# Performance work log

Measured on AMD Instinct MI355X. Metric: run time of the kernel, lower is better.

Reference implementation:

```python
import jax, jax.numpy as jnp
import numpy as np

V, I_DIM, H_DIM, NUM_CLASSES = 32000, 300, 300, 3
B, T = 64, 128


def setup_inputs() -> dict:
    key = jax.random.key(0)
    ks = jax.random.split(key, 32)
    def g(k, shape, s=0.05):
        return (jax.random.normal(k, shape, jnp.float32) * s)
    linputs = jax.random.randint(ks[0], (B, T), 0, V)
    rinputs = jax.random.randint(ks[1], (B, T), 0, V)
    # strictly-lower-triangular binary child masks (children processed before parents)
    tril = jnp.tril(jnp.ones((T, T), jnp.float32), k=-1)
    lgraph = (jax.random.uniform(ks[2], (B, T, T)) < 0.05).astype(jnp.float32) * tril
    rgraph = (jax.random.uniform(ks[3], (B, T, T)) < 0.05).astype(jnp.float32) * tril
    emb = g(ks[4], (V, I_DIM), 0.02).at[0].set(0.0)  # padding_idx=0
    names = ['wi', 'wf', 'wo', 'wu', 'ui', 'uf', 'uo', 'uu']
    params = {}
    for n, (kw, kb) in zip(names, [(ks[5 + 2 * i], ks[6 + 2 * i]) for i in range(8)]):
        params[n + '_w'] = g(kw, (H_DIM, I_DIM if n[0] == 'w' else H_DIM))
        params[n + '_b'] = g(kb, (H_DIM,))
    params['gcn_w'] = g(ks[21], (H_DIM, H_DIM))
    params['wh_w'] = g(ks[22], (H_DIM, 4 * H_DIM))
    params['wh_b'] = g(ks[23], (H_DIM,))
    params['wp_w'] = g(ks[24], (NUM_CLASSES, H_DIM))
    params['wp_b'] = g(ks[25], (NUM_CLASSES,))
    return dict(linputs=linputs, lgraph=lgraph, rinputs=rinputs, rgraph=rgraph, emb=emb, **params)


def _lin(x, w, b):
    return x @ w.T + b


def _forward(linputs, lgraph, rinputs, rgraph, emb,
             wi_w, wi_b, wf_w, wf_b, wo_w, wo_b, wu_w, wu_b,
             ui_w, ui_b, uf_w, uf_b, uo_w, uo_b, uu_w, uu_b,
             gcn_w, wh_w, wh_b, wp_w, wp_b):
    def tree_lstm(x, graph):
        Bd, Td, _ = x.shape
        # precompute input projections for all timesteps: [B,T,H]
        Xi = _lin(x, wi_w, wi_b)
        Xf = _lin(x, wf_w, wf_b)
        Xo = _lin(x, wo_w, wo_b)
        Xu = _lin(x, wu_w, wu_b)
        h0 = jnp.zeros((Bd, Td, H_DIM), x.dtype)
        c0 = jnp.zeros_like(h0)

        def step(carry, inp):
            h, c = carry
            xi, xf, xo, xu, mrow, j = inp  # xi..xu: [B,H], mrow: [B,T]
            hj = h[:, j]  # [B,H]
            i = jax.nn.sigmoid(xi + _lin(hj, ui_w, ui_b))
            o = jax.nn.sigmoid(xo + _lin(hj, uo_w, uo_b))
            u = jnp.tanh(xu + _lin(hj, uu_w, uu_b))
            f = jax.nn.sigmoid(xf[:, None, :] + _lin(h, uf_w, uf_b))  # [B,T,H]
            c_new = i * u + jnp.einsum('bt,bth->bh', mrow, f * c)
            h_new = o * jnp.tanh(c_new)
            return (h.at[:, j].set(h_new), c.at[:, j].set(c_new)), None

        xs = (jnp.swapaxes(Xi, 0, 1), jnp.swapaxes(Xf, 0, 1),
              jnp.swapaxes(Xo, 0, 1), jnp.swapaxes(Xu, 0, 1),
              jnp.swapaxes(graph, 0, 1), jnp.arange(Td))
        (h, c), _ = jax.lax.scan(step, (h0, c0), xs)
        return h, c

    def gcn(graph, h):
        Td = graph.shape[1]
        A = jnp.eye(Td, dtype=graph.dtype)[None] + jnp.swapaxes(graph, 1, 2) + graph
        return jax.nn.relu(jnp.einsum('bst,bth->bsh', A, h @ gcn_w))

    le = emb[linputs]
    re = emb[rinputs]
    lh, _ = tree_lstm(le, lgraph)
    rh, _ = tree_lstm(re, rgraph)
    ls = gcn(lgraph, lh)
    rs = gcn(rgraph, rh)
    v = jnp.concatenate([ls.max(axis=1), rs.max(axis=1), ls.mean(axis=1), rs.mean(axis=1)], axis=1)
    return _lin(jax.nn.relu(_lin(v, wh_w, wh_b)), wp_w, wp_b)


def reference(linputs, lgraph, rinputs, rgraph, emb,
              wi_w, wi_b, wf_w, wf_b, wo_w, wo_b, wu_w, wu_b,
              ui_w, ui_b, uf_w, uf_b, uo_w, uo_b, uu_w, uu_b,
              gcn_w, wh_w, wh_b, wp_w, wp_b):
    return _forward(linputs, lgraph, rinputs, rgraph, emb,
                    wi_w, wi_b, wf_w, wf_b, wo_w, wo_b, wu_w, wu_b,
                    ui_w, ui_b, uf_w, uf_b, uo_w, uo_b, uu_w, uu_b,
                    gcn_w, wh_w, wh_b, wp_w, wp_b)
```

## Files before the change

kernel.cpp:

```cpp
#include <hip/hip_runtime.h>
#include <math.h>

#define BD 64
#define TD 128
#define HD 300
#define NROW (2*BD*TD)
#define ROWSZ ((size_t)NROW*HD)
#define CMAX 32
#define AMAX 64
#define RTHREADS 960

__device__ __forceinline__ float sigf(float x){ return 1.f/(1.f+expf(-x)); }

__global__ __launch_bounds__(256) void gates_gemm_k(
    const int* __restrict__ tokL, const int* __restrict__ tokR,
    const float* __restrict__ emb,
    const float* __restrict__ wi_w, const float* __restrict__ wf_w,
    const float* __restrict__ wo_w, const float* __restrict__ wu_w,
    const float* __restrict__ wi_b, const float* __restrict__ ui_b,
    const float* __restrict__ wf_b, const float* __restrict__ uf_b,
    const float* __restrict__ wo_b, const float* __restrict__ uo_b,
    const float* __restrict__ wu_b, const float* __restrict__ uu_b,
    float* __restrict__ IU, float* __restrict__ Og, float* __restrict__ F0)
{
  __shared__ __align__(16) float As[32][64];
  __shared__ __align__(16) float Bs[4][32][64];
  const int r0 = blockIdx.x * 64;
  const int n0 = blockIdx.y * 64;
  const int tid = threadIdx.x;

  const int am  = tid >> 2;
  const int akq = tid & 3;
  const float* arow;
  {
    int r = r0 + am;
    int tree = r >> 13;
    int tok  = (tree ? tokR : tokL)[r & 8191];
    arow = emb + (size_t)tok * HD;
  }

  const float* Bm[4] = {wi_w, wf_w, wo_w, wu_w};
  const int bn  = tid >> 2;
  const int bkq = tid & 3;
  const bool nok = (n0 + bn) < HD;

  const int tm = tid >> 4;
  const int tn = tid & 15;
  float acc[4][4][4] = {};

  for (int k0 = 0; k0 < HD; k0 += 32){
    #pragma unroll
    for (int h = 0; h < 2; ++h){
      int k  = akq*8 + h*4;
      int kg = k0 + k;
      float4 v;
      if (kg + 3 < HD) v = *(const float4*)(arow + kg);
      else {
        v.x = (kg   < HD) ? arow[kg]   : 0.f;
        v.y = (kg+1 < HD) ? arow[kg+1] : 0.f;
        v.z = (kg+2 < HD) ? arow[kg+2] : 0.f;
        v.w = (kg+3 < HD) ? arow[kg+3] : 0.f;
      }
      As[k+0][am] = v.x; As[k+1][am] = v.y; As[k+2][am] = v.z; As[k+3][am] = v.w;
    }
    #pragma unroll
    for (int g = 0; g < 4; ++g){
      const float* brow = Bm[g] + (size_t)(n0 + bn) * HD;
      #pragma unroll
      for (int h = 0; h < 2; ++h){
        int k  = bkq*8 + h*4;
        int kg = k0 + k;
        float4 v = {0.f,0.f,0.f,0.f};
        if (nok){
          if (kg + 3 < HD) v = *(const float4*)(brow + kg);
          else {
            if (kg   < HD) v.x = brow[kg];
            if (kg+1 < HD) v.y = brow[kg+1];
            if (kg+2 < HD) v.z = brow[kg+2];
          }
        }
        Bs[g][k+0][bn] = v.x; Bs[g][k+1][bn] = v.y;
        Bs[g][k+2][bn] = v.z; Bs[g][k+3][bn] = v.w;
      }
    }
    __syncthreads();

    #pragma unroll 8
    for (int k = 0; k < 32; ++k){
      float a[4];
      *(float4*)a = *(const float4*)&As[k][tm*4];
      #pragma unroll
      for (int g = 0; g < 4; ++g){
        float bb[4];
        *(float4*)bb = *(const float4*)&Bs[g][k][tn*4];
        #pragma unroll
        for (int i = 0; i < 4; ++i)
          #pragma unroll
          for (int j = 0; j < 4; ++j)
            acc[g][i][j] += a[i]*bb[j];
      }
    }
    __syncthreads();
  }

  #pragma unroll
  for (int j = 0; j < 4; ++j){
    int col = n0 + tn*4 + j;
    if (col >= HD) continue;
    float bi = wi_b[col] + ui_b[col];
    float bf = wf_b[col] + uf_b[col];
    float bo = wo_b[col] + uo_b[col];
    float bu = wu_b[col] + uu_b[col];
    #pragma unroll
    for (int i = 0; i < 4; ++i){
      int r = r0 + tm*4 + i;
      size_t idx = (size_t)r * HD + col;
      float ii = sigf(acc[0][i][j] + bi);
      float uu = tanhf(acc[3][i][j] + bu);
      IU[idx] = ii * uu;
      Og[idx] = sigf(acc[2][i][j] + bo);
      F0[idx] = acc[1][i][j] + bf;
    }
  }
}

__global__ __launch_bounds__(256) void gemm_nn_k(
    const float* __restrict__ A, const float* __restrict__ B,
    float* __restrict__ C)
{
  __shared__ __align__(16) float As[32][64];
  __shared__ __align__(16) float Bs[32][64];
  const int r0 = blockIdx.x * 64;
  const int n0 = blockIdx.y * 64;
  const int tid = threadIdx.x;

  const int am  = tid >> 2;
  const int akq = tid & 3;
  const float* arow = A + (size_t)(r0 + am) * HD;

  const int tm = tid >> 4;
  const int tn = tid & 15;
  float acc[4][4] = {};

  for (int k0 = 0; k0 < HD; k0 += 32){
    #pragma unroll
    for (int h = 0; h < 2; ++h){
      int k  = akq*8 + h*4;
      int kg = k0 + k;
      float4 v;
      if (kg + 3 < HD) v = *(const float4*)(arow + kg);
      else {
        v.x = (kg   < HD) ? arow[kg]   : 0.f;
        v.y = (kg+1 < HD) ? arow[kg+1] : 0.f;
        v.z = (kg+2 < HD) ? arow[kg+2] : 0.f;
        v.w = (kg+3 < HD) ? arow[kg+3] : 0.f;
      }
      As[k+0][am] = v.x; As[k+1][am] = v.y; As[k+2][am] = v.z; As[k+3][am] = v.w;
    }
    {
      int bk  = tid >> 3;
      int bnq = tid & 7;
      int kg  = k0 + bk;
      const float* brow = B + (size_t)kg * HD;
      #pragma unroll
      for (int h = 0; h < 2; ++h){
        int n  = bnq*8 + h*4;
        int ng = n0 + n;
        float4 v = {0.f,0.f,0.f,0.f};
        if (kg < HD){
          if (ng + 3 < HD) v = *(const float4*)(brow + ng);
          else {
            if (ng   < HD) v.x = brow[ng];
            if (ng+1 < HD) v.y = brow[ng+1];
            if (ng+2 < HD) v.z = brow[ng+2];
          }
        }
        *(float4*)&Bs[bk][n] = v;
      }
    }
    __syncthreads();

    #pragma unroll 8
    for (int k = 0; k < 32; ++k){
      float a[4], bb[4];
      *(float4*)a  = *(const float4*)&As[k][tm*4];
      *(float4*)bb = *(const float4*)&Bs[k][tn*4];
      #pragma unroll
      for (int i = 0; i < 4; ++i)
        #pragma unroll
        for (int j = 0; j < 4; ++j)
          acc[i][j] += a[i]*bb[j];
    }
    __syncthreads();
  }

  #pragma unroll
  for (int i = 0; i < 4; ++i){
    int r = r0 + tm*4 + i;
    #pragma unroll
    for (int j = 0; j < 4; ++j){
      int col = n0 + tn*4 + j;
      if (col < HD) C[(size_t)r * HD + col] = acc[i][j];
    }
  }
}

__global__ __launch_bounds__(RTHREADS) void recurrence_k(
    float* IU_C,
    float* Og_H,
    float* F0_G,
    const float* __restrict__ gL, const float* __restrict__ gR,
    const float* __restrict__ ufw)
{
  const int wg   = blockIdx.x;
  const int tree = wg >> 6;
  const int b    = wg & 63;
  const float* graph = tree ? gR : gL;
  const int tid = threadIdx.x;

  __shared__ float  cw  [TD][CMAX];
  __shared__ unsigned char cidx[TD][CMAX];
  __shared__ int    ccnt[TD];
  __shared__ int    lvl [TD];
  __shared__ int    cnt [TD+1];
  __shared__ int    cur [TD+1];
  __shared__ int    lvstart[TD+1];
  __shared__ int    order[TD];
  __shared__ int    changed, nlv_s;
  __shared__ __align__(16) float hl[32][HD];
  __shared__ __align__(16) float pacc[3][8][HD];

  if (tid < TD){
    const int j = tid;
    const float* grow = graph + ((size_t)b*TD + j)*TD;
    int c = 0;
    for (int t = 0; t < j; ++t){
      float m = grow[t];
      if (m != 0.f && c < CMAX){ cidx[j][c] = (unsigned char)t; cw[j][c] = m; ++c; }
    }
    ccnt[j] = c;
    lvl[j] = 0;
  }
  __syncthreads();

  for (int it = 0; it < TD; ++it){
    if (tid == 0) changed = 0;
    __syncthreads();
    if (tid < TD){
      int m = 0, cn = ccnt[tid];
      for (int li = 0; li < cn; ++li){
        int lc = lvl[cidx[tid][li]] + 1;
        m = m > lc ? m : lc;
      }
      if (m > lvl[tid]){ lvl[tid] = m; changed = 1; }
    }
    __syncthreads();
    int ch = changed;
    __syncthreads();
    if (!ch) break;
  }

  if (tid == 0) nlv_s = 0;
  for (int q = tid; q <= TD; q += RTHREADS){ cnt[q] = 0; }
  __syncthreads();
  if (tid < TD){
    atomicMax(&nlv_s, lvl[tid] + 1);
    atomicAdd(&cnt[lvl[tid]], 1);
  }
  __syncthreads();
  const int nlv = nlv_s;
  if (tid == 0){
    int run = 0;
    for (int lv = 0; lv < nlv; ++lv){
      lvstart[lv] = run; cur[lv] = run; run += cnt[lv];
    }
    lvstart[nlv] = run;
  }
  __syncthreads();
  if (tid < TD){
    int p = atomicAdd(&cur[lvl[tid]], 1);
    order[p] = tid;
  }
  __syncthreads();

  const size_t base = (size_t)(tree*BD + b) * TD * HD;

  const int kg = tid / 320;
  const int td = tid - kg*320;

  for (int lv = 0; lv < nlv; ++lv){
    const int s = lvstart[lv], e = lvstart[lv+1];
    const bool doB = (lv != nlv - 1);
    for (int cs0 = s; cs0 < e; cs0 += 32){
      const int csn = (e - cs0) < 32 ? (e - cs0) : 32;

      for (int q = tid; q < csn*HD; q += RTHREADS){
        int ni = q / HD;
        int d  = q - ni*HD;
        int j  = order[cs0 + ni];
        size_t rj = base + (size_t)j*HD + d;
        float f0  = F0_G[rj];
        float acc = 0.f;
        const int cn = ccnt[j];
        if (cn > 0){
          int   t0 = cidx[j][0];
          float w0 = cw[j][0];
          float g0 = F0_G[base + (size_t)t0*HD + d];
          float c0 = IU_C[base + (size_t)t0*HD + d];
          for (int li = 1; li < cn; ++li){
            int   t1 = cidx[j][li];
            float w1 = cw[j][li];
            float g1 = F0_G[base + (size_t)t1*HD + d];
            float c1 = IU_C[base + (size_t)t1*HD + d];
            acc += w0 * sigf(f0 + g0) * c0;
            w0 = w1; g0 = g1; c0 = c1;
          }
          acc += w0 * sigf(f0 + g0) * c0;
        }
        float c = IU_C[rj] + acc;
        float h = Og_H[rj] * tanhf(c);
        IU_C[rj] = c; Og_H[rj] = h; hl[ni][d] = h;
      }
      __syncthreads();

      if (doB){
        for (int nb0 = 0; nb0 < csn; nb0 += 8){
          if (td < HD){
            const int d = td;
            const float4* wrow = (const float4*)(ufw + (size_t)d * HD) + kg*25;
            float acc[8];
            #pragma unroll
            for (int ni = 0; ni < 8; ++ni) acc[ni] = 0.f;
            #pragma unroll 5
            for (int k4 = 0; k4 < 25; ++k4){
              float4 w = wrow[k4];
              const int kb = kg*100 + k4*4;
              #pragma unroll
              for (int ni = 0; ni < 8; ++ni){
                float4 h4 = *(const float4*)&hl[nb0+ni][kb];
                acc[ni] += w.x*h4.x + w.y*h4.y + w.z*h4.z + w.w*h4.w;
              }
            }
            #pragma unroll
            for (int ni = 0; ni < 8; ++ni) pacc[kg][ni][d] = acc[ni];
          }
          __syncthreads();
          for (int q = tid; q < 8*HD; q += RTHREADS){
            int ni = q / HD;
            int d  = q - ni*HD;
            if (nb0 + ni < csn){
              int j = order[cs0 + nb0 + ni];
              F0_G[base + (size_t)j*HD + d] =
                  pacc[0][ni][d] + pacc[1][ni][d] + pacc[2][ni][d];
            }
          }
          __syncthreads();
        }
      } else {
        __syncthreads();
      }
    }
  }
}

__global__ __launch_bounds__(320) void gcn_pool_k(
    const float* __restrict__ HG,
    const float* __restrict__ gL, const float* __restrict__ gR,
    float* __restrict__ vbuf)
{
  const int wg   = blockIdx.x;
  const int tree = wg >> 6;
  const int b    = wg & 63;
  const float* graph = tree ? gR : gL;
  const int tid = threadIdx.x;

  __shared__ float gl[TD][TD+1];
  __shared__ float aw[TD][AMAX];
  __shared__ unsigned char ai[TD][AMAX];
  __shared__ int   acnt[TD];

  for (int q = tid; q < TD*TD; q += 320)
    gl[q >> 7][q & 127] = graph[(size_t)b*TD*TD + q];
  __syncthreads();

  if (tid < TD){
    const int s = tid;
    int c = 0;
    for (int t = 0; t < TD; ++t){
      float w = gl[s][t] + gl[t][s];
      if (w != 0.f && c < AMAX){ ai[s][c] = (unsigned char)t; aw[s][c] = w; ++c; }
    }
    acnt[s] = c;
  }
  __syncthreads();

  const size_t base = (size_t)(tree*BD + b) * TD * HD;
  if (tid < HD){
    float mx = -3.4e38f, sm = 0.f;
    for (int s = 0; s < TD; ++s){
      float v = HG[base + (size_t)s*HD + tid];
      const int cn = acnt[s];
      for (int li = 0; li < cn; ++li)
        v += aw[s][li] * HG[base + (size_t)ai[s][li]*HD + tid];
      v = fmaxf(v, 0.f);
      mx = fmaxf(mx, v);
      sm += v;
    }
    vbuf[(size_t)b*1200 + tree*HD + tid]       = mx;
    vbuf[(size_t)b*1200 + 600 + tree*HD + tid] = sm * (1.f/128.f);
  }
}

__global__ __launch_bounds__(320) void classifier_k(
    const float* __restrict__ vbuf,
    const float* __restrict__ wh_w, const float* __restrict__ wh_b,
    const float* __restrict__ wp_w, const float* __restrict__ wp_b,
    float* __restrict__ out)
{
  const int b = blockIdx.x;
  const int tid = threadIdx.x;
  __shared__ __align__(16) float vrow[1200];
  __shared__ float hid[300];
  __shared__ float red[5];

  for (int m = tid; m < 1200; m += 320) vrow[m] = vbuf[(size_t)b*1200 + m];
  __syncthreads();

  if (tid < HD){
    const float4* wrow = (const float4*)(wh_w + (size_t)tid*1200);
    float a0 = wh_b[tid], a1 = 0.f, a2 = 0.f, a3 = 0.f;
    #pragma unroll 5
    for (int m4 = 0; m4 < 300; ++m4){
      float4 w = wrow[m4];
      float4 v = *(const float4*)&vrow[m4*4];
      a0 += w.x*v.x; a1 += w.y*v.y; a2 += w.z*v.z; a3 += w.w*v.w;
    }
    hid[tid] = fmaxf((a0+a1)+(a2+a3), 0.f);
  }
  __syncthreads();

  const int wave = tid >> 6, lane = tid & 63;
  for (int n = 0; n < 3; ++n){
    float p = (tid < HD) ? wp_w[n*HD + tid] * hid[tid] : 0.f;
    #pragma unroll
    for (int off = 32; off > 0; off >>= 1) p += __shfl_down(p, off);
    if (lane == 0) red[wave] = p;
    __syncthreads();
    if (tid == 0){
      float s = wp_b[n];
      for (int wv = 0; wv < 5; ++wv) s += red[wv];
      out[(size_t)b*3 + n] = s;
    }
    __syncthreads();
  }
}

extern "C" void kernel_launch(void* const* d_in, const int* in_sizes, int n_in,
                              void* d_out, int out_size, void* d_ws, size_t ws_size,
                              hipStream_t stream) {
  const int*   linputs = (const int*)  d_in[0];
  const float* lgraph  = (const float*)d_in[1];
  const int*   rinputs = (const int*)  d_in[2];
  const float* rgraph  = (const float*)d_in[3];
  const float* emb     = (const float*)d_in[4];
  const float* wi_w = (const float*)d_in[5],  *wi_b = (const float*)d_in[6];
  const float* wf_w = (const float*)d_in[7],  *wf_b = (const float*)d_in[8];
  const float* wo_w = (const float*)d_in[9],  *wo_b = (const float*)d_in[10];
  const float* wu_w = (const float*)d_in[11], *wu_b = (const float*)d_in[12];
  const float* ui_b = (const float*)d_in[14];
  const float* uf_w = (const float*)d_in[15], *uf_b = (const float*)d_in[16];
  const float* uo_b = (const float*)d_in[18];
  const float* uu_b = (const float*)d_in[20];
  const float* gcn_w = (const float*)d_in[21];
  const float* wh_w  = (const float*)d_in[22], *wh_b = (const float*)d_in[23];
  const float* wp_w  = (const float*)d_in[24], *wp_b = (const float*)d_in[25];

  float* ws   = (float*)d_ws;
  float* buf0 = ws;
  float* buf1 = ws + 1*ROWSZ;
  float* buf2 = ws + 2*ROWSZ;
  float* vbuf = ws + 3*ROWSZ;
  float* out  = (float*)d_out;

  dim3 gg(NROW/64, 5);
  gates_gemm_k<<<gg,256,0,stream>>>(linputs, rinputs, emb,
      wi_w, wf_w, wo_w, wu_w,
      wi_b, ui_b, wf_b, uf_b, wo_b, uo_b, wu_b, uu_b,
      buf0, buf1, buf2);

  recurrence_k<<<128,RTHREADS,0,stream>>>(buf0, buf1, buf2, lgraph, rgraph, uf_w);

  gemm_nn_k<<<gg,256,0,stream>>>(buf1, gcn_w, buf0);

  gcn_pool_k<<<128,320,0,stream>>>(buf0, lgraph, rgraph, vbuf);
  classifier_k<<<64,320,0,stream>>>(vbuf, wh_w, wh_b, wp_w, wp_b, out);

  (void)in_sizes; (void)n_in; (void)out_size; (void)ws_size;
}
```

Before: 913.8 us.

## Interleave cell state and forget-gate buffers; stage graph in LDS

The gate GEMM now writes the cell input (i*u) and the forget pre-activation as interleaved float2 pairs in one buffer. The recurrence can then gather each child's c and forget term with a single 8-byte load instead of two scattered scalar loads. The child loop is unrolled by four so several gathers are in flight at once. The per-batch adjacency matrix is also copied into LDS with coalesced loads before the children are extracted, replacing per-thread strided row scans. This adds about 66KB of LDS per block, which raises the kernel's total LDS use close to the per-CU limit.

After: 919.1 us. Within noise of the previous version (+0.6%).

```diff
diff --git a/kernel.cpp b/kernel.cpp
--- a/kernel.cpp
+++ b/kernel.cpp
@@ -21,7 +21,7 @@
     const float* __restrict__ wf_b, const float* __restrict__ uf_b,
     const float* __restrict__ wo_b, const float* __restrict__ uo_b,
     const float* __restrict__ wu_b, const float* __restrict__ uu_b,
-    float* __restrict__ IU, float* __restrict__ Og, float* __restrict__ F0)
+    float* __restrict__ CG, float* __restrict__ Og)
 {
   __shared__ __align__(16) float As[32][64];
   __shared__ __align__(16) float Bs[4][32][64];
@@ -117,9 +117,9 @@
       size_t idx = (size_t)r * HD + col;
       float ii = sigf(acc[0][i][j] + bi);
       float uu = tanhf(acc[3][i][j] + bu);
-      IU[idx] = ii * uu;
+      float2 cf; cf.x = ii * uu; cf.y = acc[1][i][j] + bf;
+      *(float2*)&CG[2*idx] = cf;
       Og[idx] = sigf(acc[2][i][j] + bo);
-      F0[idx] = acc[1][i][j] + bf;
     }
   }
 }
@@ -206,9 +206,8 @@
 }
 
 __global__ __launch_bounds__(RTHREADS) void recurrence_k(
-    float* IU_C,
-    float* Og_H,
-    float* F0_G,
+    float* OgH,
+    float* CG,
     const float* __restrict__ gL, const float* __restrict__ gR,
     const float* __restrict__ ufw)
 {
@@ -218,6 +217,7 @@
   const float* graph = tree ? gR : gL;
   const int tid = threadIdx.x;
 
+  __shared__ float gl[TD][TD+1];
   __shared__ float  cw  [TD][CMAX];
   __shared__ unsigned char cidx[TD][CMAX];
   __shared__ int    ccnt[TD];
@@ -230,12 +230,15 @@
   __shared__ __align__(16) float hl[32][HD];
   __shared__ __align__(16) float pacc[3][8][HD];
 
+  for (int q = tid; q < TD*TD; q += RTHREADS)
+    gl[q >> 7][q & 127] = graph[(size_t)b*TD*TD + q];
+  __syncthreads();
+
   if (tid < TD){
     const int j = tid;
-    const float* grow = graph + ((size_t)b*TD + j)*TD;
     int c = 0;
     for (int t = 0; t < j; ++t){
-      float m = grow[t];
+      float m = gl[j][t];
       if (m != 0.f && c < CMAX){ cidx[j][c] = (unsigned char)t; cw[j][c] = m; ++c; }
     }
     ccnt[j] = c;
@@ -299,27 +302,32 @@
         int d  = q - ni*HD;
         int j  = order[cs0 + ni];
         size_t rj = base + (size_t)j*HD + d;
-        float f0  = F0_G[rj];
+        float2 fi = *(const float2*)&CG[2*rj];
+        const float f0 = fi.y;
         float acc = 0.f;
         const int cn = ccnt[j];
-        if (cn > 0){
-          int   t0 = cidx[j][0];
-          float w0 = cw[j][0];
-          float g0 = F0_G[base + (size_t)t0*HD + d];
-          float c0 = IU_C[base + (size_t)t0*HD + d];
-          for (int li = 1; li < cn; ++li){
-            int   t1 = cidx[j][li];
-            float w1 = cw[j][li];
-            float g1 = F0_G[base + (size_t)t1*HD + d];
-            float c1 = IU_C[base + (size_t)t1*HD + d];
-            acc += w0 * sigf(f0 + g0) * c0;
-            w0 = w1; g0 = g1; c0 = c1;
-          }
-          acc += w0 * sigf(f0 + g0) * c0;
+        int li = 0;
+        for (; li + 4 <= cn; li += 4){
+          int t0 = cidx[j][li+0], t1 = cidx[j][li+1];
+          int t2 = cidx[j][li+2], t3 = cidx[j][li+3];
+          float2 a0 = *(const float2*)&CG[2*(base + (size_t)t0*HD + d)];
+          float2 a1 = *(const float2*)&CG[2*(base + (size_t)t1*HD + d)];
+          float2 a2 = *(const float2*)&CG[2*(base + (size_t)t2*HD + d)];
+          float2 a3 = *(const float2*)&CG[2*(base + (size_t)t3*HD + d)];
+          acc += cw[j][li+0] * sigf(f0 + a0.y) * a0.x;
+          acc += cw[j][li+1] * sigf(f0 + a1.y) * a1.x;
+          acc += cw[j][li+2] * sigf(f0 + a2.y) * a2.x;
+          acc += cw[j][li+3] * sigf(f0 + a3.y) * a3.x;
         }
-        float c = IU_C[rj] + acc;
-        float h = Og_H[rj] * tanhf(c);
-        IU_C[rj] = c; Og_H[rj] = h; hl[ni][d] = h;
+        for (; li < cn; ++li){
+          int t = cidx[j][li];
+          float2 a = *(const float2*)&CG[2*(base + (size_t)t*HD + d)];
+          acc += cw[j][li] * sigf(f0 + a.y) * a.x;
+        }
+        float c = fi.x + acc;
+        float h = OgH[rj] * tanhf(c);
+        CG[2*rj] = c;
+        OgH[rj] = h; hl[ni][d] = h;
       }
       __syncthreads();
 
@@ -350,7 +358,7 @@
             int d  = q - ni*HD;
             if (nb0 + ni < csn){
               int j = order[cs0 + nb0 + ni];
-              F0_G[base + (size_t)j*HD + d] =
+              CG[2*(base + (size_t)j*HD + d) + 1] =
                   pacc[0][ni][d] + pacc[1][ni][d] + pacc[2][ni][d];
             }
           }
@@ -477,8 +485,8 @@
 
   float* ws   = (float*)d_ws;
   float* buf0 = ws;
-  float* buf1 = ws + 1*ROWSZ;
-  float* buf2 = ws + 2*ROWSZ;
+  float* CG   = ws + 1*ROWSZ;
+  float* HG   = ws + 1*ROWSZ;
   float* vbuf = ws + 3*ROWSZ;
   float* out  = (float*)d_out;
 
@@ -486,13 +494,13 @@
   gates_gemm_k<<<gg,256,0,stream>>>(linputs, rinputs, emb,
       wi_w, wf_w, wo_w, wu_w,
       wi_b, ui_b, wf_b, uf_b, wo_b, uo_b, wu_b, uu_b,
-      buf0, buf1, buf2);
-
-  recurrence_k<<<128,RTHREADS,0,stream>>>(buf0, buf1, buf2, lgraph, rgraph, uf_w);
-
-  gemm_nn_k<<<gg,256,0,stream>>>(buf1, gcn_w, buf0);
-
-  gcn_pool_k<<<128,320,0,stream>>>(buf0, lgraph, rgraph, vbuf);
+      CG, buf0);
+
+  recurrence_k<<<128,RTHREADS,0,stream>>>(buf0, CG, lgraph, rgraph, uf_w);
+
+  gemm_nn_k<<<gg,256,0,stream>>>(buf0, gcn_w, HG);
+
+  gcn_pool_k<<<128,320,0,stream>>>(HG, lgraph, rgraph, vbuf);
   classifier_k<<<64,320,0,stream>>>(vbuf, wh_w, wh_b, wp_w, wp_b, out);
 
   (void)in_sizes; (void)n_in; (void)out_size; (void)ws_size;
```
